# Kernel optimization log

Measured on AMD Instinct MI355X. Metric: run time of the kernel, lower is better.

## Reference

```python
import jax, jax.numpy as jnp
import numpy as np

DEPTH = 6
HIDDEN = 1152
INTER = 4304
HEADS = 16
HEAD_DIM = HIDDEN // HEADS  # 72
NUM_IMAGES = 4
GH = 32
GW = 32
MERGE = 2
SEQ = NUM_IMAGES * GH * GW  # 4096, cu_seqlens = [0,1024,2048,3072,4096]
OUT_HIDDEN = 2048
NPOS_SIDE = 48
PATCH_DIM = 3 * 2 * 16 * 16  # 1536
DS_IDX = (2, 4)
EPS = 1e-6
SCALE = HEAD_DIM ** -0.5
MERGED = HIDDEN * MERGE * MERGE  # 4608


def _block_order(h, w, m):
    # token order that groups m x m spatial-merge blocks contiguously
    return np.arange(h * w).reshape(h // m, m, w // m, m).transpose(0, 2, 1, 3).reshape(-1)

_ORDER = _block_order(GH, GW, MERGE)


def _rope_cos_sin():
    hpos = _ORDER // GW
    wpos = _ORDER % GW
    half = HEAD_DIM // 2
    inv = 1.0 / (10000.0 ** (np.arange(0, half, 2, dtype=np.float32) / half))
    fr = np.arange(max(GH, GW), dtype=np.float32)[:, None] * inv[None, :]
    r = np.concatenate([fr[hpos], fr[wpos]], axis=-1)  # (GH*GW, head_dim//2)
    emb = np.tile(np.concatenate([r, r], axis=-1), (NUM_IMAGES, 1))  # (SEQ, HEAD_DIM)
    return jnp.asarray(np.cos(emb)), jnp.asarray(np.sin(emb))


def _pos_interp():
    # static bilinear-interp gather indices/weights: 48x48 grid -> (GH,GW), block order
    n = NPOS_SIDE
    hl = np.linspace(0, n - 1, GH); wl = np.linspace(0, n - 1, GW)
    h0 = np.floor(hl).astype(np.int64); h1 = np.minimum(h0 + 1, n - 1); dh = (hl - h0).astype(np.float32)
    w0 = np.floor(wl).astype(np.int64); w1 = np.minimum(w0 + 1, n - 1); dw = (wl - w0).astype(np.float32)
    idx = np.stack([(h0[:, None] * n + w0[None, :]).reshape(-1),
                    (h0[:, None] * n + w1[None, :]).reshape(-1),
                    (h1[:, None] * n + w0[None, :]).reshape(-1),
                    (h1[:, None] * n + w1[None, :]).reshape(-1)], 0)
    wgt = np.stack([((1 - dh)[:, None] * (1 - dw)[None, :]).reshape(-1),
                    ((1 - dh)[:, None] * dw[None, :]).reshape(-1),
                    (dh[:, None] * (1 - dw)[None, :]).reshape(-1),
                    (dh[:, None] * dw[None, :]).reshape(-1)], 0).astype(np.float32)
    return idx[:, _ORDER], wgt[:, _ORDER]

_PIDX, _PWGT = _pos_interp()


def _ln(x, g, b):
    mu = x.mean(-1, keepdims=True)
    var = ((x - mu) ** 2).mean(-1, keepdims=True)
    return (x - mu) * jax.lax.rsqrt(var + EPS) * g + b


def _rot_half(x):
    x1, x2 = jnp.split(x, 2, axis=-1)
    return jnp.concatenate([-x2, x1], axis=-1)


def _attention(x, qkv_w, qkv_b, proj_w, proj_b, cos, sin):
    qkv = (x @ qkv_w.T + qkv_b).reshape(SEQ, 3, HEADS, HEAD_DIM)
    q, k, v = qkv[:, 0], qkv[:, 1], qkv[:, 2]
    c, s = cos[:, None, :], sin[:, None, :]
    q = q * c + _rot_half(q) * s
    k = k * c + _rot_half(k) * s
    # equal-length cu_seqlens chunks -> batched block-diagonal attention
    qb = q.reshape(NUM_IMAGES, -1, HEADS, HEAD_DIM)
    kb = k.reshape(NUM_IMAGES, -1, HEADS, HEAD_DIM)
    vb = v.reshape(NUM_IMAGES, -1, HEADS, HEAD_DIM)
    att = jax.nn.softmax(jnp.einsum('bqhd,bkhd->bhqk', qb, kb) * SCALE, axis=-1)
    o = jnp.einsum('bhqk,bkhd->bqhd', att, vb).reshape(SEQ, HIDDEN)
    return o @ proj_w.T + proj_b


def _merger(x, g, b, f1w, f1b, f2w, f2b, post):
    if post:
        h = _ln(x.reshape(-1, MERGED), g, b)
    else:
        h = _ln(x, g, b).reshape(-1, MERGED)
    h = jax.nn.gelu(h @ f1w.T + f1b, approximate=True)
    return h @ f2w.T + f2b


def setup_inputs():
    key = jax.random.key(0)
    ks = iter(jax.random.split(key, 40))
    def w(shape, scale=0.02):
        return jax.random.normal(next(ks), shape, jnp.float32) * scale
    return {
        'pixel_values': jax.random.normal(next(ks), (SEQ, PATCH_DIM), jnp.float32),
        'patch_w': w((HIDDEN, PATCH_DIM)), 'patch_b': w((HIDDEN,)),
        'pos_embed': w((NPOS_SIDE * NPOS_SIDE, HIDDEN)),
        'qkv_w': w((DEPTH, 3 * HIDDEN, HIDDEN)), 'qkv_b': w((DEPTH, 3 * HIDDEN)),
        'proj_w': w((DEPTH, HIDDEN, HIDDEN)), 'proj_b': w((DEPTH, HIDDEN)),
        'ln1_g': jnp.ones((DEPTH, HIDDEN)), 'ln1_b': jnp.zeros((DEPTH, HIDDEN)),
        'ln2_g': jnp.ones((DEPTH, HIDDEN)), 'ln2_b': jnp.zeros((DEPTH, HIDDEN)),
        'fc1_w': w((DEPTH, INTER, HIDDEN)), 'fc1_b': w((DEPTH, INTER)),
        'fc2_w': w((DEPTH, HIDDEN, INTER)), 'fc2_b': w((DEPTH, HIDDEN)),
        'm_ln_g': jnp.ones((HIDDEN,)), 'm_ln_b': jnp.zeros((HIDDEN,)),
        'm_fc1_w': w((MERGED, MERGED)), 'm_fc1_b': w((MERGED,)),
        'm_fc2_w': w((OUT_HIDDEN, MERGED)), 'm_fc2_b': w((OUT_HIDDEN,)),
        'ds_ln_g': jnp.ones((2, MERGED)), 'ds_ln_b': jnp.zeros((2, MERGED)),
        'ds_fc1_w': w((2, MERGED, MERGED)), 'ds_fc1_b': w((2, MERGED)),
        'ds_fc2_w': w((2, OUT_HIDDEN, MERGED)), 'ds_fc2_b': w((2, OUT_HIDDEN)),
    }


def reference(pixel_values, patch_w, patch_b, pos_embed, qkv_w, qkv_b, proj_w, proj_b,
              ln1_g, ln1_b, ln2_g, ln2_b, fc1_w, fc1_b, fc2_w, fc2_b,
              m_ln_g, m_ln_b, m_fc1_w, m_fc1_b, m_fc2_w, m_fc2_b,
              ds_ln_g, ds_ln_b, ds_fc1_w, ds_fc1_b, ds_fc2_w, ds_fc2_b):
    cos, sin = _rope_cos_sin()
    # patch embed: stride==kernel Conv3d == flat linear on (C*T*P*P)
    x = pixel_values @ patch_w.T + patch_b  # (SEQ, HIDDEN)
    pe = (pos_embed[jnp.asarray(_PIDX)] * jnp.asarray(_PWGT)[..., None]).sum(0)
    x = x + jnp.tile(pe, (NUM_IMAGES, 1))
    ds = []
    for i in range(DEPTH):
        x = x + _attention(_ln(x, ln1_g[i], ln1_b[i]), qkv_w[i], qkv_b[i], proj_w[i], proj_b[i], cos, sin)
        h = _ln(x, ln2_g[i], ln2_b[i])
        x = x + (jax.nn.gelu(h @ fc1_w[i].T + fc1_b[i], approximate=True) @ fc2_w[i].T + fc2_b[i])
        if i in DS_IDX:
            j = DS_IDX.index(i)
            ds.append(_merger(x, ds_ln_g[j], ds_ln_b[j], ds_fc1_w[j], ds_fc1_b[j], ds_fc2_w[j], ds_fc2_b[j], post=True))
    out = _merger(x, m_ln_g, m_ln_b, m_fc1_w, m_fc1_b, m_fc2_w, m_fc2_b, post=False)
    return (out, ds[0], ds[1])
```

## Files before the change

### kernel.cpp

```cpp
#include <hip/hip_runtime.h>
#include <hip/hip_bf16.h>
#include <math.h>

typedef __hip_bfloat16 bf16;
typedef __attribute__((ext_vector_type(8))) __bf16 bfv8;
typedef __attribute__((ext_vector_type(4))) __bf16 bfv4;
typedef __attribute__((ext_vector_type(4))) float float4v;

__device__ inline float bf2f(bf16 v) { return __bfloat162float(v); }
__device__ inline bf16 f2bf(float v) { return __float2bfloat16(v); }

__device__ inline float gelu_f(float v) {
  return 0.5f * v * (1.f + tanhf(0.7978845608028654f * (v + 0.044715f * v * v * v)));
}

__global__ void dtype_probe(const unsigned* __restrict__ g, int* __restrict__ flag) {
  *flag = (*g == 0x3F800000u) ? 1 : 0;
}

__device__ inline float loadf_dyn(const void* p, long i, int isf32) {
  return isf32 ? ((const float*)p)[i] : bf2f(((const bf16*)p)[i]);
}

__global__ __launch_bounds__(256) void cvt_bf16(const void* __restrict__ src,
                                                long off, __bf16* __restrict__ dst,
                                                long n, const int* __restrict__ flagp) {
  const long i = ((long)blockIdx.x * 256 + threadIdx.x) * 8;
  if (i >= n) return;
  if (*flagp) {
    const float* sp = (const float*)src + off + i;
    float4v a = *(const float4v*)sp;
    float4v b = *(const float4v*)(sp + 4);
    bfv8 r;
    r[0] = (__bf16)a[0]; r[1] = (__bf16)a[1];
    r[2] = (__bf16)a[2]; r[3] = (__bf16)a[3];
    r[4] = (__bf16)b[0]; r[5] = (__bf16)b[1];
    r[6] = (__bf16)b[2]; r[7] = (__bf16)b[3];
    *(bfv8*)(dst + i) = r;
  } else {
    *(bfv8*)(dst + i) = *(const bfv8*)((const __bf16*)src + off + i);
  }
}

__device__ inline void cp16(const __bf16* g, __bf16* l) {
  __builtin_amdgcn_global_load_lds(
      (const __attribute__((address_space(1))) void*)g,
      (__attribute__((address_space(3))) void*)l, 16, 0, 0);
}

template <int EPI>
__global__ __launch_bounds__(256) void gemm_bt(
    const void* __restrict__ Av, const void* __restrict__ Wv,
    const void* __restrict__ Bv, void* __restrict__ Cv,
    const int* __restrict__ flagp, int M, int N, int K, int lda, int ldw,
    int ldc, long sA, long sW, long sC, long a0, long w0, long b0, long c0,
    int ksplit, int zheads, long slabC, float scale) {
  __shared__ __align__(16) __bf16 As[2][128 * 32];
  __shared__ __align__(16) __bf16 Ws[2][128 * 32];
  const int tid = threadIdx.x;
  const int bz = blockIdx.z;

  const int nx = gridDim.x;
  const int nwg = nx * gridDim.y;
  const int orig = blockIdx.y * nx + blockIdx.x;
  const int xcd = orig & 7, lid = orig >> 3, qq = nwg >> 3, rr = nwg & 7;
  const int wg = (xcd < rr ? xcd * (qq + 1) : rr * (qq + 1) + (xcd - rr) * qq) + lid;
  const int bm = (wg / nx) * 128;
  const int bn = (wg % nx) * 128;

  int head = bz, ks = 0, kof = 0, klen = K;
  if (ksplit > 0) {
    head = bz % zheads;
    ks = bz / zheads;
    kof = ks * ksplit;
    klen = min(ksplit, K - kof);
  }
  const __bf16* Ap = (const __bf16*)Av + a0 + (size_t)head * sA + kof;
  const __bf16* Wp = (const __bf16*)Wv + w0 + (size_t)head * sW + kof;

  const int lane = tid & 63, wid = tid >> 6;
  const int wm = (wid >> 1) * 64, wn = (wid & 1) * 64;
  const int q = lane >> 4, lm = lane & 15;

  const int sr = lane >> 2;
  const int sc = (lane & 3) * 8;
  const int ar = bm + wid * 32 + sr;
  const int wr = bn + wid * 32 + sr;
  const size_t aoff0 = (size_t)(ar < M ? ar : M - 1) * lda + sc;
  const size_t aoff1 = (size_t)(ar + 16 < M ? ar + 16 : M - 1) * lda + sc;
  const size_t woff0 = (size_t)(wr < N ? wr : N - 1) * ldw + sc;
  const size_t woff1 = (size_t)(wr + 16 < N ? wr + 16 : N - 1) * ldw + sc;

  float4v acc[4][4];
#pragma unroll
  for (int i = 0; i < 4; i++)
#pragma unroll
    for (int j = 0; j < 4; j++) acc[i][j] = (float4v)0.f;

  const int nfull = klen >> 5;
  const int kr = klen & 31;

  auto stage = [&](int buf, int kt) {
    const int k0 = kt << 5;
    __bf16* lA = &As[buf][wid * 1024];
    __bf16* lW = &Ws[buf][wid * 1024];
    cp16(Ap + aoff0 + k0, lA);
    cp16(Ap + aoff1 + k0, lA + 512);
    cp16(Wp + woff0 + k0, lW);
    cp16(Wp + woff1 + k0, lW + 512);
  };
  auto stage_tail = [&](int buf) {
    const int k0 = nfull << 5;
    const int r0 = tid >> 2, ce = (tid & 3) * 8;
#pragma unroll
    for (int it = 0; it < 2; ++it) {
      const int r = r0 + it * 64;
      const int gm = bm + r, gn = bn + r;
      bfv8 av = (bfv8)(__bf16)0.f;
      if (ce < kr && gm < M) av = *(const bfv8*)(Ap + (size_t)gm * lda + k0 + ce);
      *(bfv8*)&As[buf][r * 32 + ce] = av;
      bfv8 wv = (bfv8)(__bf16)0.f;
      if (ce < kr && gn < N) wv = *(const bfv8*)(Wp + (size_t)gn * ldw + k0 + ce);
      *(bfv8*)&Ws[buf][r * 32 + ce] = wv;
    }
  };
  auto compute = [&](int buf) {
    bfv8 af[4], wf[4];
#pragma unroll
    for (int i = 0; i < 4; i++) {
      af[i] = *(const bfv8*)&As[buf][(wm + i * 16 + lm) * 32 + q * 8];
      wf[i] = *(const bfv8*)&Ws[buf][(wn + i * 16 + lm) * 32 + q * 8];
    }
    __builtin_amdgcn_s_setprio(1);
#pragma unroll
    for (int i = 0; i < 4; i++)
#pragma unroll
      for (int j = 0; j < 4; j++)
        acc[i][j] = __builtin_amdgcn_mfma_f32_16x16x32_bf16(af[i], wf[j],
                                                            acc[i][j], 0, 0, 0);
    __builtin_amdgcn_s_setprio(0);
  };

  int cur = 0;
  if (nfull > 0) stage(0, 0);
  else if (kr) stage_tail(0);
  __syncthreads();
  for (int kt = 0; kt < nfull; ++kt) {
    if (kt + 1 < nfull) stage(cur ^ 1, kt + 1);
    else if (kr) stage_tail(cur ^ 1);
    compute(cur);
    __syncthreads();
    cur ^= 1;
  }
  if (kr) compute(cur);

  const int isf32 = *flagp;
  float* Cf = (float*)Cv;
  bf16* Cb = (bf16*)Cv;
  const size_t cbase = (size_t)c0 + (size_t)head * sC + (size_t)ks * slabC;
#pragma unroll
  for (int i = 0; i < 4; i++) {
#pragma unroll
    for (int j = 0; j < 4; j++) {
      const int col = bn + wn + j * 16 + lm;
      if (col >= N) continue;
      float bv = 0.f;
      if (EPI != 4 && Bv) bv = loadf_dyn(Bv, b0 + col, isf32);
#pragma unroll
      for (int r = 0; r < 4; r++) {
        const int rowg = bm + wm + i * 16 + q * 4 + r;
        if (rowg >= M) continue;
        float v = acc[i][j][r] + bv;
        const size_t off = cbase + (size_t)rowg * ldc + col;
        if (EPI == 0) {
          Cb[off] = f2bf(v);
        } else if (EPI == 1) {
          Cb[off] = f2bf(gelu_f(v));
        } else if (EPI == 3) {
          Cf[off] = v;
        } else if (EPI == 4) {
          Cf[off] = v * scale;
        }
      }
    }
  }
}

template <int MODE>
__global__ __launch_bounds__(256) void reduce_add(
    const float* __restrict__ part, long slab, int S,
    const void* __restrict__ bias, long b0, void* __restrict__ outv, long c0,
    long n, int N, const int* __restrict__ flagp) {
  const int isf32 = *flagp;
  const long i4 = ((long)blockIdx.x * 256 + threadIdx.x) * 4;
  if (i4 >= n) return;
  float4v s = *(const float4v*)(part + i4);
  for (int t = 1; t < S; ++t) s += *(const float4v*)(part + (size_t)t * slab + i4);
  if (MODE == 4) {
    const long z = i4 / 73728;
    const long rem = i4 % 73728;
    const long row = rem / 72;
    const long col = rem % 72;
    bfv4 r;
#pragma unroll
    for (int u = 0; u < 4; ++u) r[u] = (__bf16)s[u];
    *(bfv4*)((bf16*)outv + row * 1152 + z * 72 + col) = r;
    return;
  }
  const int col = (int)(i4 % N);
#pragma unroll
  for (int u = 0; u < 4; ++u) s[u] += loadf_dyn(bias, b0 + col + u, isf32);
  if (MODE == 0) {
    *(float4v*)((float*)outv + i4) = s;
  } else if (MODE == 1) {
    float4v x0 = *(const float4v*)((float*)outv + i4);
    *(float4v*)((float*)outv + i4) = x0 + s;
  } else if (MODE == 2) {
    bfv4 r;
#pragma unroll
    for (int u = 0; u < 4; ++u) r[u] = (__bf16)gelu_f(s[u]);
    *(bfv4*)((bf16*)outv + i4) = r;
  } else {
    if (isf32) {
      *(float4v*)((float*)outv + c0 + i4) = s;
    } else {
      bfv4 r;
#pragma unroll
      for (int u = 0; u < 4; ++u) r[u] = (__bf16)s[u];
      *(bfv4*)((bf16*)outv + c0 + i4) = r;
    }
  }
}

__global__ __launch_bounds__(256) void ln_rows(const float* __restrict__ x,
                                               const void* __restrict__ g,
                                               const void* __restrict__ b,
                                               long gboff, bf16* __restrict__ out,
                                               int C, const int* __restrict__ flagp) {
  const int isf32 = *flagp;
  const int row = blockIdx.x;
  const float* xp = x + (size_t)row * C;
  const int tid = threadIdx.x;
  float s = 0.f, ss = 0.f;
  for (int c = tid; c < C; c += 256) {
    float v = xp[c];
    s += v;
    ss += v * v;
  }
#pragma unroll
  for (int off = 32; off >= 1; off >>= 1) {
    s += __shfl_xor(s, off);
    ss += __shfl_xor(ss, off);
  }
  __shared__ float rs_[4], rss_[4];
  const int wid = tid >> 6;
  if ((tid & 63) == 0) {
    rs_[wid] = s;
    rss_[wid] = ss;
  }
  __syncthreads();
  s = rs_[0] + rs_[1] + rs_[2] + rs_[3];
  ss = rss_[0] + rss_[1] + rss_[2] + rss_[3];
  const float mu = s / C;
  const float var = ss / C - mu * mu;
  const float rstd = rsqrtf(var + 1e-6f);
  bf16* op = out + (size_t)row * C;
  for (int c = tid; c < C; c += 256)
    op[c] = f2bf((xp[c] - mu) * rstd * loadf_dyn(g, gboff + c, isf32) +
                 loadf_dyn(b, gboff + c, isf32));
}

__global__ __launch_bounds__(256) void pe_add(const void* __restrict__ pos,
                                              float* __restrict__ x,
                                              const int* __restrict__ flagp) {
  const int isf32 = *flagp;
  const int idx = blockIdx.x * 256 + threadIdx.x;
  const int h = idx % 1152;
  const int p = idx / 1152;
  const int j = p & 1, i2 = (p >> 1) & 1, bw = (p >> 2) & 15, bh = p >> 6;
  const int hpos = bh * 2 + i2, wpos = bw * 2 + j;
  const double hv = hpos * 47.0 / 31.0, wv = wpos * 47.0 / 31.0;
  const int h0 = (int)hv, w0 = (int)wv;
  const int h1 = min(h0 + 1, 47), w1 = min(w0 + 1, 47);
  const float dh = (float)(hv - h0), dw = (float)(wv - w0);
  const float pe =
      (1.f - dh) * (1.f - dw) * loadf_dyn(pos, (long)(h0 * 48 + w0) * 1152 + h, isf32) +
      (1.f - dh) * dw * loadf_dyn(pos, (long)(h0 * 48 + w1) * 1152 + h, isf32) +
      dh * (1.f - dw) * loadf_dyn(pos, (long)(h1 * 48 + w0) * 1152 + h, isf32) +
      dh * dw * loadf_dyn(pos, (long)(h1 * 48 + w1) * 1152 + h, isf32);
#pragma unroll
  for (int img = 0; img < 4; ++img)
    x[((size_t)(img * 1024 + p)) * 1152 + h] += pe;
}

__global__ __launch_bounds__(256) void rope_split(const bf16* __restrict__ qkv,
                                                  bf16* __restrict__ qb,
                                                  bf16* __restrict__ kb,
                                                  bf16* __restrict__ vt) {
  const int idx = blockIdx.x * 256 + threadIdx.x;
  const int d = idx % 72;
  const int sh = idx / 72;
  const int hh = sh & 15;
  const int s = sh >> 4;
  const int p = s & 1023, img = s >> 10;
  const int jj = p & 1, ii = (p >> 1) & 1, bw = (p >> 2) & 15, bh = p >> 6;
  const int hpos = 2 * bh + ii, wpos = 2 * bw + jj;
  const int dd = (d < 36) ? d : d - 36;
  int t, posv;
  if (dd < 18) { t = dd; posv = hpos; }
  else { t = dd - 18; posv = wpos; }
  const float ang = posv * powf(10000.f, -(2.f * t) / 36.f);
  const float c = cosf(ang), sn = sinf(ang);
  const size_t base = (size_t)s * 3456 + hh * 72;
  const int d2 = (d < 36) ? d + 36 : d - 36;
  const float qv = bf2f(qkv[base + d]);
  const float q2 = bf2f(qkv[base + d2]);
  const float kv = bf2f(qkv[base + 1152 + d]);
  const float k2 = bf2f(qkv[base + 1152 + d2]);
  const float qr = (d < 36) ? qv * c - q2 * sn : qv * c + q2 * sn;
  const float kr = (d < 36) ? kv * c - k2 * sn : kv * c + k2 * sn;
  const size_t ob = (size_t)s * 1152 + hh * 72 + d;
  qb[ob] = f2bf(qr);
  kb[ob] = f2bf(kr);
  vt[(((size_t)(img * 16 + hh)) * 72 + d) * 1024 + p] = qkv[base + 2304 + d];
}

__global__ __launch_bounds__(256) void softmax_rows(const float* __restrict__ S,
                                                    bf16* __restrict__ P) {
  const size_t row = blockIdx.x;
  const float* sp = S + row * 1024;
  const int tid = threadIdx.x;
  float v[4];
  float m = -1e30f;
#pragma unroll
  for (int i = 0; i < 4; i++) {
    v[i] = sp[tid + (i << 8)];
    m = fmaxf(m, v[i]);
  }
#pragma unroll
  for (int off = 32; off >= 1; off >>= 1) m = fmaxf(m, __shfl_xor(m, off));
  __shared__ float red[8];
  const int wid = tid >> 6;
  if ((tid & 63) == 0) red[wid] = m;
  __syncthreads();
  m = fmaxf(fmaxf(red[0], red[1]), fmaxf(red[2], red[3]));
  float s = 0.f;
#pragma unroll
  for (int i = 0; i < 4; i++) {
    v[i] = expf(v[i] - m);
    s += v[i];
  }
#pragma unroll
  for (int off = 32; off >= 1; off >>= 1) s += __shfl_xor(s, off);
  if ((tid & 63) == 0) red[4 + wid] = s;
  __syncthreads();
  s = red[4] + red[5] + red[6] + red[7];
  const float inv = 1.f / s;
  bf16* pp = P + row * 1024;
#pragma unroll
  for (int i = 0; i < 4; i++) pp[tid + (i << 8)] = f2bf(v[i] * inv);
}

extern "C" void kernel_launch(void* const* d_in, const int* in_sizes, int n_in,
                              void* d_out, int out_size, void* d_ws,
                              size_t ws_size, hipStream_t stream) {
  const void* pixel = d_in[0];
  const void* patch_w = d_in[1];
  const void* patch_b = d_in[2];
  const void* pos_emb = d_in[3];
  const void* qkv_w = d_in[4];
  const void* qkv_b = d_in[5];
  const void* proj_w = d_in[6];
  const void* proj_b = d_in[7];
  const void* ln1_g = d_in[8];
  const void* ln1_b = d_in[9];
  const void* ln2_g = d_in[10];
  const void* ln2_b = d_in[11];
  const void* fc1_w = d_in[12];
  const void* fc1_b = d_in[13];
  const void* fc2_w = d_in[14];
  const void* fc2_b = d_in[15];
  const void* m_ln_g = d_in[16];
  const void* m_ln_b = d_in[17];
  const void* m_fc1_w = d_in[18];
  const void* m_fc1_b = d_in[19];
  const void* m_fc2_w = d_in[20];
  const void* m_fc2_b = d_in[21];
  const void* ds_ln_g = d_in[22];
  const void* ds_ln_b = d_in[23];
  const void* ds_fc1_w = d_in[24];
  const void* ds_fc1_b = d_in[25];
  const void* ds_fc2_w = d_in[26];
  const void* ds_fc2_b = d_in[27];

  char* wp = (char*)d_ws;
  auto alloc = [&](size_t bytes) -> char* {
    char* r = wp;
    wp += (bytes + 255) & ~(size_t)255;
    return r;
  };
  int* flag = (int*)alloc(256);
  float* x = (float*)alloc(4718592ull * 4);
  bf16* a_bf = (bf16*)alloc(4718592ull * 2);
  bf16* qkvb = (bf16*)alloc(14155776ull * 2);
  bf16* qb = (bf16*)alloc(4718592ull * 2);
  bf16* kb = (bf16*)alloc(4718592ull * 2);
  bf16* vt = (bf16*)alloc(4718592ull * 2);
  bf16* o_bf = (bf16*)alloc(4718592ull * 2);
  float* sbuf = (float*)alloc(16777216ull * 4);
  bf16* h_bf = (bf16*)alloc(17629184ull * 2);
  bf16* p_bf = h_bf;
  __bf16* wcv = (__bf16*)sbuf;
  __bf16* pix_bf = wcv;
  __bf16* pw_bf = wcv + 8388608;
  float* part = (float*)qkvb;
  const long SLAB = 4718592;

  const dim3 blk(256);
  auto gg = [](int N, int M, int S) {
    return dim3((unsigned)((N + 127) / 128), (unsigned)((M + 127) / 128), (unsigned)S);
  };
  auto cvt = [&](const void* s, long off, __bf16* d, long n) {
    cvt_bf16<<<dim3((unsigned)((n / 8 + 255) / 256)), blk, 0, stream>>>(s, off, d, n, flag);
  };
  auto rgrid = [](long n) { return dim3((unsigned)((n / 4 + 255) / 256)); };
  const float SCALE = 0.11785113019775793f;

  dtype_probe<<<1, 1, 0, stream>>>((const unsigned*)ln1_g, flag);

  cvt(pixel, 0, pix_bf, 6291456);
  cvt(patch_w, 0, pw_bf, 1769472);
  gemm_bt<3><<<gg(1152, 4096, 3), blk, 0, stream>>>(
      pix_bf, pw_bf, nullptr, part, flag, 4096, 1152, 1536, 1536, 1536, 1152,
      0, 0, 0, 0, 0, 0, 0, 512, 1, SLAB, 1.f);
  reduce_add<0><<<rgrid(4718592), blk, 0, stream>>>(
      part, SLAB, 3, patch_b, 0, (void*)x, 0, 4718592, 1152, flag);
  pe_add<<<4608, 256, 0, stream>>>(pos_emb, x, flag);

  for (long L = 0; L < 6; ++L) {
    ln_rows<<<4096, 256, 0, stream>>>(x, ln1_g, ln1_b, L * 1152, a_bf, 1152, flag);
    cvt(qkv_w, L * 3981312L, wcv, 3981312);
    gemm_bt<0><<<gg(3456, 4096, 1), blk, 0, stream>>>(
        a_bf, wcv, qkv_b, qkvb, flag, 4096, 3456, 1152, 1152, 1152, 3456, 0,
        0, 0, 0, 0, L * 3456, 0, 0, 1, 0, 1.f);
    rope_split<<<18432, 256, 0, stream>>>(qkvb, qb, kb, vt);
    for (int img = 0; img < 4; ++img) {
      gemm_bt<4><<<dim3(8, 8, 16), blk, 0, stream>>>(
          qb + (size_t)img * 1179648, kb + (size_t)img * 1179648, nullptr,
          (void*)sbuf, flag, 1024, 1024, 72, 1152, 1152, 1024, 72, 72, 1048576,
          0, 0, 0, 0, 0, 1, 0, SCALE);
      softmax_rows<<<16384, 256, 0, stream>>>(sbuf, p_bf);
      gemm_bt<3><<<dim3(1, 8, 64), blk, 0, stream>>>(
          p_bf, vt + (size_t)img * 1179648, nullptr, part, flag, 1024, 72,
          1024, 1024, 1024, 72, 1048576, 73728, 73728, 0, 0, 0, 0, 256, 16,
          1179648, 1.f);
      reduce_add<4><<<rgrid(1179648), blk, 0, stream>>>(
          part, 1179648, 4, nullptr, 0, (void*)(o_bf + (size_t)img * 1179648),
          0, 1179648, 72, flag);
    }
    cvt(proj_w, L * 1327104L, wcv, 1327104);
    gemm_bt<3><<<gg(1152, 4096, 3), blk, 0, stream>>>(
        o_bf, wcv, nullptr, part, flag, 4096, 1152, 1152, 1152, 1152, 1152,
        0, 0, 0, 0, 0, 0, 0, 384, 1, SLAB, 1.f);
    reduce_add<1><<<rgrid(4718592), blk, 0, stream>>>(
        part, SLAB, 3, proj_b, L * 1152, (void*)x, 0, 4718592, 1152, flag);

    ln_rows<<<4096, 256, 0, stream>>>(x, ln2_g, ln2_b, L * 1152, a_bf, 1152, flag);
    cvt(fc1_w, L * 4958208L, wcv, 4958208);
    gemm_bt<1><<<gg(4304, 4096, 1), blk, 0, stream>>>(
        a_bf, wcv, fc1_b, h_bf, flag, 4096, 4304, 1152, 1152, 1152, 4304, 0,
        0, 0, 0, 0, L * 4304, 0, 0, 1, 0, 1.f);
    cvt(fc2_w, L * 4958208L, wcv, 4958208);
    gemm_bt<3><<<gg(1152, 4096, 3), blk, 0, stream>>>(
        h_bf, wcv, nullptr, part, flag, 4096, 1152, 4304, 4304, 4304, 1152,
        0, 0, 0, 0, 0, 0, 0, 1440, 1, SLAB, 1.f);
    reduce_add<1><<<rgrid(4718592), blk, 0, stream>>>(
        part, SLAB, 3, fc2_b, L * 1152, (void*)x, 0, 4718592, 1152, flag);

    if (L == 2 || L == 4) {
      const long j = (L == 2) ? 0 : 1;
      ln_rows<<<1024, 256, 0, stream>>>(x, ds_ln_g, ds_ln_b, j * 4608, a_bf, 4608, flag);
      cvt(ds_fc1_w, j * 21233664L, wcv, 21233664);
      gemm_bt<3><<<gg(4608, 1024, 3), blk, 0, stream>>>(
          a_bf, wcv, nullptr, part, flag, 1024, 4608, 4608, 4608, 4608, 4608,
          0, 0, 0, 0, 0, 0, 0, 1536, 1, SLAB, 1.f);
      reduce_add<2><<<rgrid(4718592), blk, 0, stream>>>(
          part, SLAB, 3, ds_fc1_b, j * 4608, h_bf, 0, 4718592, 4608, flag);
      cvt(ds_fc2_w, j * 9437184L, wcv, 9437184);
      gemm_bt<3><<<gg(2048, 1024, 4), blk, 0, stream>>>(
          h_bf, wcv, nullptr, part, flag, 1024, 2048, 4608, 4608, 4608, 2048,
          0, 0, 0, 0, 0, 0, 0, 1152, 1, 2097152, 1.f);
      reduce_add<3><<<rgrid(2097152), blk, 0, stream>>>(
          part, 2097152, 4, ds_fc2_b, j * 2048, d_out, (1 + j) * 2097152L,
          2097152, 2048, flag);
    }
  }
  ln_rows<<<4096, 256, 0, stream>>>(x, m_ln_g, m_ln_b, 0, a_bf, 1152, flag);
  cvt(m_fc1_w, 0, wcv, 21233664);
  gemm_bt<3><<<gg(4608, 1024, 3), blk, 0, stream>>>(
      a_bf, wcv, nullptr, part, flag, 1024, 4608, 4608, 4608, 4608, 4608,
      0, 0, 0, 0, 0, 0, 0, 1536, 1, SLAB, 1.f);
  reduce_add<2><<<rgrid(4718592), blk, 0, stream>>>(
      part, SLAB, 3, m_fc1_b, 0, h_bf, 0, 4718592, 4608, flag);
  cvt(m_fc2_w, 0, wcv, 9437184);
  gemm_bt<3><<<gg(2048, 1024, 4), blk, 0, stream>>>(
      h_bf, wcv, nullptr, part, flag, 1024, 2048, 4608, 4608, 4608, 2048,
      0, 0, 0, 0, 0, 0, 0, 1152, 1, 2097152, 1.f);
  reduce_add<3><<<rgrid(2097152), blk, 0, stream>>>(
      part, 2097152, 4, m_fc2_b, 0, d_out, 0, 2097152, 2048, flag);
}
```

Baseline: 5.063 ms.

## Fuse attention into a flash-style kernel with online softmax

Replaces the per-image sequence of QK^T GEMM, the row softmax over a materialized fp32 score buffer, the split-K PV GEMM and its reduction with one fused kernel. The new kernel keeps a 64-row query tile in shared memory, streams 128-key K/V tiles, and computes the softmax online with running max and sum. Q/K are padded to 96 columns with zeros so the MFMA K-loop is aligned, and the softmax scale is folded into Q during RoPE. This removes the large score-matrix traffic and most launches, but adds several block-wide barriers per key tile and redundant padded MFMA work.

```diff
diff --git a/kernel.cpp b/kernel.cpp
--- a/kernel.cpp
+++ b/kernel.cpp
@@ -186,6 +186,164 @@
   }
 }
 
+__global__ __launch_bounds__(256) void attn_fused(
+    const bf16* __restrict__ qbp_, const bf16* __restrict__ kbp_,
+    const bf16* __restrict__ vtp_, bf16* __restrict__ o) {
+  __shared__ __align__(16) __bf16 Qs[64 * 104];
+  __shared__ __align__(16) __bf16 Ks[128 * 104];
+  __shared__ __align__(16) __bf16 Vs[72 * 136];
+  __shared__ __align__(16) __bf16 Ps[64 * 136];
+  __shared__ float pmax[2][64], psum[2][64], mrow[64], lrow[64], srow[64];
+
+  const int tid = threadIdx.x;
+  const int lane = tid & 63, wid = tid >> 6;
+  const int q = lane >> 4, lm = lane & 15;
+  const int qt = blockIdx.x;
+  const int h = blockIdx.y;
+  const int img = blockIdx.z;
+
+  const __bf16* qp = (const __bf16*)qbp_ + ((size_t)(img * 1024 + qt * 64)) * 1536 + h * 96;
+  const __bf16* kp = (const __bf16*)kbp_ + ((size_t)(img * 1024)) * 1536 + h * 96;
+  const __bf16* vp = (const __bf16*)vtp_ + ((size_t)(img * 16 + h)) * 72 * 1024;
+
+  for (int c = tid; c < 768; c += 256) {
+    const int row = c / 12, c8 = c % 12;
+    *(bfv8*)&Qs[row * 104 + c8 * 8] =
+        *(const bfv8*)(qp + (size_t)row * 1536 + c8 * 8);
+  }
+  if (tid < 64) {
+    mrow[tid] = -1e30f;
+    lrow[tid] = 0.f;
+  }
+
+  const int wm = (wid >> 1) * 32, wn = (wid & 1) * 64;
+
+  float4v oacc[5];
+#pragma unroll
+  for (int j = 0; j < 5; j++) oacc[j] = (float4v)0.f;
+
+  for (int kt = 0; kt < 8; ++kt) {
+    __syncthreads();
+    for (int c = tid; c < 1536; c += 256) {
+      const int row = c / 12, c8 = c % 12;
+      *(bfv8*)&Ks[row * 104 + c8 * 8] =
+          *(const bfv8*)(kp + (size_t)(kt * 128 + row) * 1536 + c8 * 8);
+    }
+    for (int c = tid; c < 1152; c += 256) {
+      const int row = c >> 4, c8 = c & 15;
+      *(bfv8*)&Vs[row * 136 + c8 * 8] =
+          *(const bfv8*)(vp + (size_t)row * 1024 + kt * 128 + c8 * 8);
+    }
+    __syncthreads();
+
+    float4v sa[2][4];
+#pragma unroll
+    for (int i = 0; i < 2; i++)
+#pragma unroll
+      for (int j = 0; j < 4; j++) sa[i][j] = (float4v)0.f;
+#pragma unroll
+    for (int ks = 0; ks < 3; ks++) {
+      const int k0 = ks * 32;
+      bfv8 af[2], kf[4];
+#pragma unroll
+      for (int i = 0; i < 2; i++)
+        af[i] = *(const bfv8*)&Qs[(wm + i * 16 + lm) * 104 + k0 + q * 8];
+#pragma unroll
+      for (int j = 0; j < 4; j++)
+        kf[j] = *(const bfv8*)&Ks[(wn + j * 16 + lm) * 104 + k0 + q * 8];
+      __builtin_amdgcn_s_setprio(1);
+#pragma unroll
+      for (int i = 0; i < 2; i++)
+#pragma unroll
+        for (int j = 0; j < 4; j++)
+          sa[i][j] = __builtin_amdgcn_mfma_f32_16x16x32_bf16(af[i], kf[j],
+                                                             sa[i][j], 0, 0, 0);
+      __builtin_amdgcn_s_setprio(0);
+    }
+
+#pragma unroll
+    for (int i = 0; i < 2; i++)
+#pragma unroll
+      for (int r = 0; r < 4; r++) {
+        float mv = fmaxf(fmaxf(sa[i][0][r], sa[i][1][r]),
+                         fmaxf(sa[i][2][r], sa[i][3][r]));
+#pragma unroll
+        for (int mk = 1; mk <= 8; mk <<= 1) mv = fmaxf(mv, __shfl_xor(mv, mk));
+        if (lm == 0) pmax[wid & 1][wm + i * 16 + q * 4 + r] = mv;
+      }
+    __syncthreads();
+
+#pragma unroll
+    for (int i = 0; i < 2; i++)
+#pragma unroll
+      for (int r = 0; r < 4; r++) {
+        const int row = wm + i * 16 + q * 4 + r;
+        const float mn = fmaxf(mrow[row], fmaxf(pmax[0][row], pmax[1][row]));
+        float acc = 0.f;
+#pragma unroll
+        for (int j = 0; j < 4; j++) {
+          const float pv = __expf(sa[i][j][r] - mn);
+          acc += pv;
+          Ps[row * 136 + wn + j * 16 + lm] = (__bf16)pv;
+        }
+#pragma unroll
+        for (int mk = 1; mk <= 8; mk <<= 1) acc += __shfl_xor(acc, mk);
+        if (lm == 0) psum[wid & 1][row] = acc;
+      }
+    __syncthreads();
+
+    if (tid < 64) {
+      const float m_old = mrow[tid];
+      const float mn = fmaxf(m_old, fmaxf(pmax[0][tid], pmax[1][tid]));
+      const float sc = __expf(m_old - mn);
+      lrow[tid] = lrow[tid] * sc + psum[0][tid] + psum[1][tid];
+      mrow[tid] = mn;
+      srow[tid] = sc;
+    }
+    __syncthreads();
+
+    float scv[4];
+#pragma unroll
+    for (int r = 0; r < 4; r++) scv[r] = srow[wid * 16 + q * 4 + r];
+#pragma unroll
+    for (int j = 0; j < 5; j++)
+#pragma unroll
+      for (int r = 0; r < 4; r++) oacc[j][r] *= scv[r];
+    const int prow = (wid * 16 + lm) * 136;
+    int vro[5];
+#pragma unroll
+    for (int j = 0; j < 5; j++) {
+      const int vr = j * 16 + lm;
+      vro[j] = (vr < 72 ? vr : 71) * 136;
+    }
+#pragma unroll
+    for (int kk = 0; kk < 4; kk++) {
+      const bfv8 pf = *(const bfv8*)&Ps[prow + kk * 32 + q * 8];
+      __builtin_amdgcn_s_setprio(1);
+#pragma unroll
+      for (int j = 0; j < 5; j++) {
+        const bfv8 vf = *(const bfv8*)&Vs[vro[j] + kk * 32 + q * 8];
+        oacc[j] = __builtin_amdgcn_mfma_f32_16x16x32_bf16(pf, vf, oacc[j], 0, 0, 0);
+      }
+      __builtin_amdgcn_s_setprio(0);
+    }
+  }
+
+  float linv[4];
+#pragma unroll
+  for (int r = 0; r < 4; r++) linv[r] = 1.f / lrow[wid * 16 + q * 4 + r];
+#pragma unroll
+  for (int j = 0; j < 5; j++) {
+    const int d = j * 16 + lm;
+    if (d >= 72) continue;
+#pragma unroll
+    for (int r = 0; r < 4; r++) {
+      const size_t rowg = (size_t)(img * 1024 + qt * 64 + wid * 16 + q * 4 + r);
+      o[rowg * 1152 + h * 72 + d] = f2bf(oacc[j][r] * linv[r]);
+    }
+  }
+}
+
 template <int MODE>
 __global__ __launch_bounds__(256) void reduce_add(
     const float* __restrict__ part, long slab, int S,
@@ -196,17 +354,6 @@
   if (i4 >= n) return;
   float4v s = *(const float4v*)(part + i4);
   for (int t = 1; t < S; ++t) s += *(const float4v*)(part + (size_t)t * slab + i4);
-  if (MODE == 4) {
-    const long z = i4 / 73728;
-    const long rem = i4 % 73728;
-    const long row = rem / 72;
-    const long col = rem % 72;
-    bfv4 r;
-#pragma unroll
-    for (int u = 0; u < 4; ++u) r[u] = (__bf16)s[u];
-    *(bfv4*)((bf16*)outv + row * 1152 + z * 72 + col) = r;
-    return;
-  }
   const int col = (int)(i4 % N);
 #pragma unroll
   for (int u = 0; u < 4; ++u) s[u] += loadf_dyn(bias, b0 + col + u, isf32);
@@ -298,10 +445,16 @@
                                                   bf16* __restrict__ kb,
                                                   bf16* __restrict__ vt) {
   const int idx = blockIdx.x * 256 + threadIdx.x;
-  const int d = idx % 72;
-  const int sh = idx / 72;
+  const int d = idx % 96;
+  const int sh = idx / 96;
   const int hh = sh & 15;
   const int s = sh >> 4;
+  const size_t ob = (size_t)s * 1536 + hh * 96 + d;
+  if (d >= 72) {
+    qb[ob] = f2bf(0.f);
+    kb[ob] = f2bf(0.f);
+    return;
+  }
   const int p = s & 1023, img = s >> 10;
   const int jj = p & 1, ii = (p >> 1) & 1, bw = (p >> 2) & 15, bh = p >> 6;
   const int hpos = 2 * bh + ii, wpos = 2 * bw + jj;
@@ -319,46 +472,9 @@
   const float k2 = bf2f(qkv[base + 1152 + d2]);
   const float qr = (d < 36) ? qv * c - q2 * sn : qv * c + q2 * sn;
   const float kr = (d < 36) ? kv * c - k2 * sn : kv * c + k2 * sn;
-  const size_t ob = (size_t)s * 1152 + hh * 72 + d;
-  qb[ob] = f2bf(qr);
+  qb[ob] = f2bf(qr * 0.11785113019775793f);
   kb[ob] = f2bf(kr);
   vt[(((size_t)(img * 16 + hh)) * 72 + d) * 1024 + p] = qkv[base + 2304 + d];
-}
-
-__global__ __launch_bounds__(256) void softmax_rows(const float* __restrict__ S,
-                                                    bf16* __restrict__ P) {
-  const size_t row = blockIdx.x;
-  const float* sp = S + row * 1024;
-  const int tid = threadIdx.x;
-  float v[4];
-  float m = -1e30f;
-#pragma unroll
-  for (int i = 0; i < 4; i++) {
-    v[i] = sp[tid + (i << 8)];
-    m = fmaxf(m, v[i]);
-  }
-#pragma unroll
-  for (int off = 32; off >= 1; off >>= 1) m = fmaxf(m, __shfl_xor(m, off));
-  __shared__ float red[8];
-  const int wid = tid >> 6;
-  if ((tid & 63) == 0) red[wid] = m;
-  __syncthreads();
-  m = fmaxf(fmaxf(red[0], red[1]), fmaxf(red[2], red[3]));
-  float s = 0.f;
-#pragma unroll
-  for (int i = 0; i < 4; i++) {
-    v[i] = expf(v[i] - m);
-    s += v[i];
-  }
-#pragma unroll
-  for (int off = 32; off >= 1; off >>= 1) s += __shfl_xor(s, off);
-  if ((tid & 63) == 0) red[4 + wid] = s;
-  __syncthreads();
-  s = red[4] + red[5] + red[6] + red[7];
-  const float inv = 1.f / s;
-  bf16* pp = P + row * 1024;
-#pragma unroll
-  for (int i = 0; i < 4; i++) pp[tid + (i << 8)] = f2bf(v[i] * inv);
 }
 
 extern "C" void kernel_launch(void* const* d_in, const int* in_sizes, int n_in,
@@ -403,14 +519,12 @@
   float* x = (float*)alloc(4718592ull * 4);
   bf16* a_bf = (bf16*)alloc(4718592ull * 2);
   bf16* qkvb = (bf16*)alloc(14155776ull * 2);
-  bf16* qb = (bf16*)alloc(4718592ull * 2);
-  bf16* kb = (bf16*)alloc(4718592ull * 2);
+  bf16* qb = (bf16*)alloc(6291456ull * 2);
+  bf16* kb = (bf16*)alloc(6291456ull * 2);
   bf16* vt = (bf16*)alloc(4718592ull * 2);
   bf16* o_bf = (bf16*)alloc(4718592ull * 2);
-  float* sbuf = (float*)alloc(16777216ull * 4);
+  __bf16* wcv = (__bf16*)alloc(21233664ull * 2);
   bf16* h_bf = (bf16*)alloc(17629184ull * 2);
-  bf16* p_bf = h_bf;
-  __bf16* wcv = (__bf16*)sbuf;
   __bf16* pix_bf = wcv;
   __bf16* pw_bf = wcv + 8388608;
   float* part = (float*)qkvb;
@@ -424,7 +538,6 @@
     cvt_bf16<<<dim3((unsigned)((n / 8 + 255) / 256)), blk, 0, stream>>>(s, off, d, n, flag);
   };
   auto rgrid = [](long n) { return dim3((unsigned)((n / 4 + 255) / 256)); };
-  const float SCALE = 0.11785113019775793f;
 
   dtype_probe<<<1, 1, 0, stream>>>((const unsigned*)ln1_g, flag);
 
@@ -443,21 +556,9 @@
     gemm_bt<0><<<gg(3456, 4096, 1), blk, 0, stream>>>(
         a_bf, wcv, qkv_b, qkvb, flag, 4096, 3456, 1152, 1152, 1152, 3456, 0,
         0, 0, 0, 0, L * 3456, 0, 0, 1, 0, 1.f);
-    rope_split<<<18432, 256, 0, stream>>>(qkvb, qb, kb, vt);
-    for (int img = 0; img < 4; ++img) {
-      gemm_bt<4><<<dim3(8, 8, 16), blk, 0, stream>>>(
-          qb + (size_t)img * 1179648, kb + (size_t)img * 1179648, nullptr,
-          (void*)sbuf, flag, 1024, 1024, 72, 1152, 1152, 1024, 72, 72, 1048576,
-          0, 0, 0, 0, 0, 1, 0, SCALE);
-      softmax_rows<<<16384, 256, 0, stream>>>(sbuf, p_bf);
-      gemm_bt<3><<<dim3(1, 8, 64), blk, 0, stream>>>(
-          p_bf, vt + (size_t)img * 1179648, nullptr, part, flag, 1024, 72,
-          1024, 1024, 1024, 72, 1048576, 73728, 73728, 0, 0, 0, 0, 256, 16,
-          1179648, 1.f);
-      reduce_add<4><<<rgrid(1179648), blk, 0, stream>>>(
-          part, 1179648, 4, nullptr, 0, (void*)(o_bf + (size_t)img * 1179648),
-          0, 1179648, 72, flag);
-    }
+    rope_split<<<24576, 256, 0, stream>>>(qkvb, qb, kb, vt);
+    attn_fused<<<dim3(16, 16, 4), blk, 0, stream>>>(qb, kb, vt, o_bf);
+
     cvt(proj_w, L * 1327104L, wcv, 1327104);
     gemm_bt<3><<<gg(1152, 4096, 3), blk, 0, stream>>>(
         o_bf, wcv, nullptr, part, flag, 4096, 1152, 1152, 1152, 1152, 1152,
```

Result: faster. 4.499 ms (-11.1%).
